# Optimization experiments

Measured on AMD Instinct MI355X. Metric: run time of the kernel, lower is better.

The kernel has to match this reference:

```python
import jax, jax.numpy as jnp
import numpy as np


def _gcn_layer(x, W, b, row, col, num_nodes):
    # x: [N, F_in]; W: [F_in, F_out]; row/col: [E2] (with self-loops appended)
    xw = x @ W  # [N, F_out]
    ones = jnp.ones(row.shape[0], dtype=xw.dtype)
    deg = jax.ops.segment_sum(ones, col, num_segments=num_nodes)  # in-degree incl. self-loop
    dinv = jnp.where(deg > 0, jax.lax.rsqrt(deg), 0.0)
    norm = dinv[row] * dinv[col]  # [E2]
    msg = xw[row] * norm[:, None]  # gather + per-edge scale
    out = jax.ops.segment_sum(msg, col, num_segments=num_nodes)  # scatter-add to targets
    return out + b


def setup_inputs() -> dict:
    key = jax.random.key(0)
    k1, k2, k3, k4, k5 = jax.random.split(key, 5)
    N, E, F_in, F_hid = 100000, 640000, 128, 128
    x = jax.random.normal(k1, (N, F_in), dtype=jnp.float32)
    edge_index = jax.random.randint(k2, (2, E), 0, N, dtype=jnp.int64)
    # Glorot-style init like PyG GCNConv
    s1 = (6.0 / (F_in + F_hid)) ** 0.5
    W1 = jax.random.uniform(k3, (F_in, F_hid), jnp.float32, -s1, s1)
    b1 = jnp.zeros((F_hid,), jnp.float32)
    s2 = (6.0 / (F_hid + F_hid)) ** 0.5
    W2 = jax.random.uniform(k4, (F_hid, F_hid), jnp.float32, -s2, s2)
    b2 = jnp.zeros((F_hid,), jnp.float32)
    return {"x": x, "edge_index": edge_index, "W1": W1, "b1": b1, "W2": W2, "b2": b2}


def reference(x, edge_index, W1, b1, W2, b2):
    N = x.shape[0]
    # GCN adds self-loops before symmetric normalization (add_self_loops=True default)
    self_idx = jnp.arange(N, dtype=edge_index.dtype)
    row = jnp.concatenate([edge_index[0], self_idx])
    col = jnp.concatenate([edge_index[1], self_idx])
    h = _gcn_layer(x, W1, b1, row, col, N)
    h = jax.nn.relu(h)
    # dropout is identity in eval mode (training=False)
    out = _gcn_layer(h, W2, b2, row, col, N)
    return out
```

## Files before the change

kernel.cpp:

```cpp
#include <hip/hip_runtime.h>
#include <cstdint>
#include <cstddef>


typedef unsigned int u32;
typedef unsigned short u16;
typedef __attribute__((ext_vector_type(8))) short short8;
typedef __attribute__((ext_vector_type(4))) float f32x4;

__device__ __forceinline__ float bf2f(u32 lo16) {
  union { u32 u; float f; } c; c.u = lo16 << 16; return c.f;
}
__device__ __forceinline__ u32 f2bf(float f) {
  union { float f; u32 u; } c; c.f = f;
  return (c.u + 0x7fffu + ((c.u >> 16) & 1u)) >> 16;
}

__global__ __launch_bounds__(256) void zero_i32_kernel(int* __restrict__ p, int n) {
  int i = blockIdx.x * 256 + threadIdx.x;
  if (i < n) p[i] = 0;
}

__global__ __launch_bounds__(256) void count_kernel(
    const int* __restrict__ cols, const int* __restrict__ rows,
    int* __restrict__ cnt, int E, int N) {
  int e = blockIdx.x * 256 + threadIdx.x;
  if (e >= E) return;
  int c = cols[e];
  int r = rows[e];
  if ((unsigned)c >= (unsigned)N || (unsigned)r >= (unsigned)N) return;
  atomicAdd(&cnt[c], 1);
}

__global__ __launch_bounds__(256) void wt_kernel(
    const float* __restrict__ W1, const float* __restrict__ W2,
    u16* __restrict__ Wt1, u16* __restrict__ Wt2) {
  int b = blockIdx.x;
  const float* W = (b < 64) ? W1 : W2;
  u16* Wt = (b < 64) ? Wt1 : Wt2;
  int idx = (b & 63) * 256 + threadIdx.x;
  int k = idx >> 7, n = idx & 127;
  Wt[n * 128 + k] = (u16)f2bf(W[idx]);
}

__global__ __launch_bounds__(256) void scan1_kernel(
    const int* __restrict__ cnt, int* __restrict__ rowptr,
    int* __restrict__ bsum, float* __restrict__ dinv, int N) {
  __shared__ int sd[256];
  int t = threadIdx.x;
  int base = blockIdx.x * 1024 + t * 4;
  int c0 = (base + 0 < N) ? cnt[base + 0] : 0;
  int c1 = (base + 1 < N) ? cnt[base + 1] : 0;
  int c2 = (base + 2 < N) ? cnt[base + 2] : 0;
  int c3 = (base + 3 < N) ? cnt[base + 3] : 0;
  if (base + 0 < N) dinv[base + 0] = rsqrtf((float)c0 + 1.0f);
  if (base + 1 < N) dinv[base + 1] = rsqrtf((float)c1 + 1.0f);
  if (base + 2 < N) dinv[base + 2] = rsqrtf((float)c2 + 1.0f);
  if (base + 3 < N) dinv[base + 3] = rsqrtf((float)c3 + 1.0f);
  int s = c0 + c1 + c2 + c3;
  sd[t] = s;
  __syncthreads();
  for (int off = 1; off < 256; off <<= 1) {
    int v = (t >= off) ? sd[t - off] : 0;
    __syncthreads();
    sd[t] += v;
    __syncthreads();
  }
  int excl = sd[t] - s;
  if (base + 0 < N) rowptr[base + 0] = excl;
  if (base + 1 < N) rowptr[base + 1] = excl + c0;
  if (base + 2 < N) rowptr[base + 2] = excl + c0 + c1;
  if (base + 3 < N) rowptr[base + 3] = excl + c0 + c1 + c2;
  if (t == 255) bsum[blockIdx.x] = sd[255];
}

__global__ __launch_bounds__(128) void scan2_kernel(
    const int* __restrict__ bsum, int* __restrict__ bsum2,
    int* __restrict__ rowptr, int NB, int N) {
  __shared__ int sd[128];
  int t = threadIdx.x;
  int v = (t < NB) ? bsum[t] : 0;
  sd[t] = v;
  __syncthreads();
  for (int off = 1; off < 128; off <<= 1) {
    int u = (t >= off) ? sd[t - off] : 0;
    __syncthreads();
    sd[t] += u;
    __syncthreads();
  }
  bsum2[t] = sd[t] - v;
  if (t == NB - 1) rowptr[N] = sd[t];
}

__global__ __launch_bounds__(256) void scan3_kernel(
    int* __restrict__ rowptr, const int* __restrict__ bsum2, int N) {
  int t = threadIdx.x;
  int b = blockIdx.x;
  int base = b * 1024 + t * 4;
  int add = bsum2[b];
#pragma unroll
  for (int k = 0; k < 4; k++)
    if (base + k < N) rowptr[base + k] += add;
}

__global__ __launch_bounds__(256) void fill_kernel(
    const int* __restrict__ cols, const int* __restrict__ rows,
    const int* __restrict__ rowptr, int* __restrict__ cnt,
    int* __restrict__ adj, int E, int N) {
  int e = blockIdx.x * 256 + threadIdx.x;
  if (e >= E) return;
  int c = cols[e];
  int r = rows[e];
  if ((unsigned)c >= (unsigned)N || (unsigned)r >= (unsigned)N) return;
  int pos = atomicSub(&cnt[c], 1) - 1;
  if (pos >= 0) adj[rowptr[c] + pos] = r;
}

template <int A_BF16>
__global__ __launch_bounds__(256) void gemm_mfma_kernel(
    const void* __restrict__ Av, const u16* __restrict__ Wt,
    const float* __restrict__ dinv, u16* __restrict__ C, int M) {
  __shared__ u16 Ws[128][136];
  __shared__ float dv_s[128];
  const int tid = threadIdx.x;
  const int row0 = blockIdx.x * 128;

  {
    const uint4* src = (const uint4*)Wt;
#pragma unroll
    for (int i = 0; i < 8; i++) {
      int linear = tid + i * 256;
      int n = linear >> 4;
      int kq = linear & 15;
      *(uint4*)&Ws[n][kq * 8] = src[linear];
    }
  }
  if (tid < 128) {
    int gr = row0 + tid;
    dv_s[tid] = (gr < M) ? dinv[gr] : 0.f;
  }
  __syncthreads();

  const int wave = tid >> 6;
  const int lane = tid & 63;
  const int lm = lane & 15;
  const int quad = lane >> 4;
  const int m0 = wave * 32;

  f32x4 acc[2][8];
#pragma unroll
  for (int mt = 0; mt < 2; mt++)
#pragma unroll
    for (int nt = 0; nt < 8; nt++) acc[mt][nt] = (f32x4){0.f, 0.f, 0.f, 0.f};

#pragma unroll
  for (int k0 = 0; k0 < 128; k0 += 32) {
    short8 bfrag[8];
#pragma unroll
    for (int nt = 0; nt < 8; nt++)
      bfrag[nt] = *(const short8*)&Ws[nt * 16 + lm][k0 + quad * 8];

    short8 afrag[2];
#pragma unroll
    for (int mt = 0; mt < 2; mt++) {
      int gr = row0 + m0 + mt * 16 + lm;
      short8 f = (short8){0, 0, 0, 0, 0, 0, 0, 0};
      if (gr < M) {
        if (A_BF16) {
          f = *(const short8*)((const u16*)Av + (size_t)gr * 128 + k0 + quad * 8);
        } else {
          const float* Af = (const float*)Av + (size_t)gr * 128 + k0 + quad * 8;
          float4 v0 = *(const float4*)Af;
          float4 v1 = *(const float4*)(Af + 4);
          f[0] = (short)f2bf(v0.x); f[1] = (short)f2bf(v0.y);
          f[2] = (short)f2bf(v0.z); f[3] = (short)f2bf(v0.w);
          f[4] = (short)f2bf(v1.x); f[5] = (short)f2bf(v1.y);
          f[6] = (short)f2bf(v1.z); f[7] = (short)f2bf(v1.w);
        }
      }
      afrag[mt] = f;
    }

#pragma unroll
    for (int mt = 0; mt < 2; mt++)
#pragma unroll
      for (int nt = 0; nt < 8; nt++)
        acc[mt][nt] = __builtin_amdgcn_mfma_f32_16x16x32_bf16(
            afrag[mt], bfrag[nt], acc[mt][nt], 0, 0, 0);
  }

  __syncthreads();
#pragma unroll
  for (int mt = 0; mt < 2; mt++) {
    int rbase = m0 + mt * 16 + quad * 4;
#pragma unroll
    for (int r = 0; r < 4; r++) {
      int lrow = rbase + r;
      float dv = dv_s[lrow];
#pragma unroll
      for (int nt = 0; nt < 8; nt++)
        Ws[lrow][nt * 16 + lm] = (u16)f2bf(acc[mt][nt][r] * dv);
    }
  }
  __syncthreads();
#pragma unroll
  for (int i = 0; i < 8; i++) {
    int linear = tid + i * 256;
    int row = linear >> 4;
    int c8 = linear & 15;
    int grow = row0 + row;
    if (grow < M)
      *(uint4*)(C + (size_t)grow * 128 + c8 * 8) = *(const uint4*)&Ws[row][c8 * 8];
  }
}

template <int RELU, int OUT_BF16>
__global__ __launch_bounds__(256) void aggregate_kernel(
    const uint4* __restrict__ xws, const int* __restrict__ rowptr,
    const int* __restrict__ adj, const float* __restrict__ dinv,
    const float* __restrict__ bias, void* __restrict__ out, int N) {
  int node = blockIdx.x * 16 + (threadIdx.x >> 4);
  if (node >= N) return;
  int lane = threadIdx.x & 15;

  float a[8];
  {
    uint4 sv = xws[(size_t)node * 16 + lane];
    a[0] = bf2f(sv.x & 0xffff); a[1] = bf2f(sv.x >> 16);
    a[2] = bf2f(sv.y & 0xffff); a[3] = bf2f(sv.y >> 16);
    a[4] = bf2f(sv.z & 0xffff); a[5] = bf2f(sv.z >> 16);
    a[6] = bf2f(sv.w & 0xffff); a[7] = bf2f(sv.w >> 16);
  }

  int beg = rowptr[node];
  int end = rowptr[node + 1];
  for (int j = beg; j < end; j += 8) {
    int sidx[8];
    float msk[8];
#pragma unroll
    for (int k = 0; k < 8; k++) {
      int jj = j + k;
      int s = (jj < end) ? adj[jj] : -1;
      float m = 1.f;
      if ((unsigned)s >= (unsigned)N) { s = 0; m = 0.f; }
      sidx[k] = s;
      msk[k] = m;
    }
    uint4 v[8];
#pragma unroll
    for (int k = 0; k < 8; k++) v[k] = xws[(size_t)sidx[k] * 16 + lane];
#pragma unroll
    for (int k = 0; k < 8; k++) {
      a[0] = fmaf(msk[k], bf2f(v[k].x & 0xffff), a[0]);
      a[1] = fmaf(msk[k], bf2f(v[k].x >> 16), a[1]);
      a[2] = fmaf(msk[k], bf2f(v[k].y & 0xffff), a[2]);
      a[3] = fmaf(msk[k], bf2f(v[k].y >> 16), a[3]);
      a[4] = fmaf(msk[k], bf2f(v[k].z & 0xffff), a[4]);
      a[5] = fmaf(msk[k], bf2f(v[k].z >> 16), a[5]);
      a[6] = fmaf(msk[k], bf2f(v[k].w & 0xffff), a[6]);
      a[7] = fmaf(msk[k], bf2f(v[k].w >> 16), a[7]);
    }
  }

  float di = dinv[node];
  float4 b0 = ((const float4*)bias)[lane * 2];
  float4 b1 = ((const float4*)bias)[lane * 2 + 1];
  float o[8];
  o[0] = fmaf(di, a[0], b0.x); o[1] = fmaf(di, a[1], b0.y);
  o[2] = fmaf(di, a[2], b0.z); o[3] = fmaf(di, a[3], b0.w);
  o[4] = fmaf(di, a[4], b1.x); o[5] = fmaf(di, a[5], b1.y);
  o[6] = fmaf(di, a[6], b1.z); o[7] = fmaf(di, a[7], b1.w);
  if (RELU) {
#pragma unroll
    for (int k = 0; k < 8; k++) o[k] = fmaxf(o[k], 0.f);
  }
  if (OUT_BF16) {
    uint4 p;
    p.x = f2bf(o[0]) | (f2bf(o[1]) << 16);
    p.y = f2bf(o[2]) | (f2bf(o[3]) << 16);
    p.z = f2bf(o[4]) | (f2bf(o[5]) << 16);
    p.w = f2bf(o[6]) | (f2bf(o[7]) << 16);
    ((uint4*)out)[(size_t)node * 16 + lane] = p;
  } else {
    float4* op = (float4*)out + (size_t)node * 32 + lane * 2;
    op[0] = make_float4(o[0], o[1], o[2], o[3]);
    op[1] = make_float4(o[4], o[5], o[6], o[7]);
  }
}

extern "C" void kernel_launch(void* const* d_in, const int* in_sizes, int n_in,
                              void* d_out, int out_size, void* d_ws, size_t ws_size,
                              hipStream_t stream) {
  const float* x  = (const float*)d_in[0];
  const int*   ei = (const int*)d_in[1];
  const float* W1 = (const float*)d_in[2];
  const float* b1 = (const float*)d_in[3];
  const float* W2 = (const float*)d_in[4];
  const float* b2 = (const float*)d_in[5];
  float* out = (float*)d_out;

  const int F = 128;
  const int N = in_sizes[0] / F;
  const int E = in_sizes[1] / 2;
  const int* rows = ei;
  const int* cols = ei + E;

  u16*   bufXW  = (u16*)d_ws;
  u16*   bufH   = bufXW + (size_t)N * F;
  float* dinv   = (float*)(bufH + (size_t)N * F);
  int*   cnt    = (int*)(dinv + N);
  int*   rowptr = cnt + N;
  int*   adj    = rowptr + (N + 1);
  int*   bsum   = adj + E;
  int*   bsum2  = bsum + 128;
  u16*   Wt1    = (u16*)(bsum2 + 128);
  u16*   Wt2    = Wt1 + 128 * 128;

  const int NB = (N + 1023) / 1024;
  int eblocks = (E + 255) / 256;
  int nblocks = (N + 255) / 256;

  zero_i32_kernel<<<nblocks, 256, 0, stream>>>(cnt, N);
  count_kernel<<<eblocks, 256, 0, stream>>>(cols, rows, cnt, E, N);
  wt_kernel<<<128, 256, 0, stream>>>(W1, W2, Wt1, Wt2);
  scan1_kernel<<<NB, 256, 0, stream>>>(cnt, rowptr, bsum, dinv, N);
  scan2_kernel<<<1, 128, 0, stream>>>(bsum, bsum2, rowptr, NB, N);
  scan3_kernel<<<NB, 256, 0, stream>>>(rowptr, bsum2, N);
  fill_kernel<<<eblocks, 256, 0, stream>>>(cols, rows, rowptr, cnt, adj, E, N);

  int gblocks = (N + 127) / 128;
  int ablocks = (N + 15) / 16;
  gemm_mfma_kernel<0><<<gblocks, 256, 0, stream>>>(x, Wt1, dinv, bufXW, N);
  aggregate_kernel<1, 1><<<ablocks, 256, 0, stream>>>(
      (const uint4*)bufXW, rowptr, adj, dinv, b1, bufH, N);
  gemm_mfma_kernel<1><<<gblocks, 256, 0, stream>>>(bufH, Wt2, dinv, bufXW, N);
  aggregate_kernel<0, 0><<<ablocks, 256, 0, stream>>>(
      (const uint4*)bufXW, rowptr, adj, dinv, b2, out, N);
}
```

Baseline: 261.9 us.

## Sort nodes into degree buckets before aggregation to balance warp work

Adds a degree histogram, a bucket scan and a counting-sort permutation so the aggregate kernels process nodes grouped by in-degree (capped at 31). Neighbouring 16-lane groups in a wavefront then have similar loop trip counts, which cuts divergence and idle lanes in the gather loop. The cost is three extra small kernel launches. Output rows are also written and self-features read in permuted order, which loses some locality for the output and self-row accesses.

```diff
diff --git a/kernel.cpp b/kernel.cpp
--- a/kernel.cpp
+++ b/kernel.cpp
@@ -76,9 +76,10 @@
 
 __global__ __launch_bounds__(128) void scan2_kernel(
     const int* __restrict__ bsum, int* __restrict__ bsum2,
-    int* __restrict__ rowptr, int NB, int N) {
+    int* __restrict__ rowptr, int* __restrict__ hist, int NB, int N) {
   __shared__ int sd[128];
   int t = threadIdx.x;
+  if (t < 32) hist[t] = 0;
   int v = (t < NB) ? bsum[t] : 0;
   sd[t] = v;
   __syncthreads();
@@ -114,6 +115,51 @@
   if ((unsigned)c >= (unsigned)N || (unsigned)r >= (unsigned)N) return;
   int pos = atomicSub(&cnt[c], 1) - 1;
   if (pos >= 0) adj[rowptr[c] + pos] = r;
+}
+
+__global__ __launch_bounds__(256) void hist_kernel(
+    const int* __restrict__ rowptr, int* __restrict__ hist, int N) {
+  __shared__ int lh[32];
+  int t = threadIdx.x;
+  if (t < 32) lh[t] = 0;
+  __syncthreads();
+  int i = blockIdx.x * 256 + t;
+  if (i < N) {
+    int deg = rowptr[i + 1] - rowptr[i];
+    int bin = deg < 31 ? deg : 31;
+    atomicAdd(&lh[bin], 1);
+  }
+  __syncthreads();
+  if (t < 32 && lh[t] > 0) atomicAdd(&hist[t], lh[t]);
+}
+
+__global__ __launch_bounds__(64) void binscan_kernel(
+    const int* __restrict__ hist, int* __restrict__ bincur) {
+  if (threadIdx.x == 0) {
+    int acc = 0;
+    for (int b = 0; b < 32; b++) { bincur[b] = acc; acc += hist[b]; }
+  }
+}
+
+__global__ __launch_bounds__(256) void perm_kernel(
+    const int* __restrict__ rowptr, int* __restrict__ bincur,
+    int* __restrict__ perm, int N) {
+  __shared__ int lh[32];
+  __shared__ int lbase[32];
+  int t = threadIdx.x;
+  if (t < 32) lh[t] = 0;
+  __syncthreads();
+  int i = blockIdx.x * 256 + t;
+  int bin = 0, lpos = 0;
+  if (i < N) {
+    int deg = rowptr[i + 1] - rowptr[i];
+    bin = deg < 31 ? deg : 31;
+    lpos = atomicAdd(&lh[bin], 1);
+  }
+  __syncthreads();
+  if (t < 32) lbase[t] = (lh[t] > 0) ? atomicAdd(&bincur[t], lh[t]) : 0;
+  __syncthreads();
+  if (i < N) perm[lbase[bin] + lpos] = i;
 }
 
 template <int A_BF16>
@@ -218,9 +264,12 @@
 __global__ __launch_bounds__(256) void aggregate_kernel(
     const uint4* __restrict__ xws, const int* __restrict__ rowptr,
     const int* __restrict__ adj, const float* __restrict__ dinv,
-    const float* __restrict__ bias, void* __restrict__ out, int N) {
-  int node = blockIdx.x * 16 + (threadIdx.x >> 4);
-  if (node >= N) return;
+    const float* __restrict__ bias, const int* __restrict__ perm,
+    void* __restrict__ out, int N) {
+  int idx = blockIdx.x * 16 + (threadIdx.x >> 4);
+  if (idx >= N) return;
+  int node = perm[idx];
+  if ((unsigned)node >= (unsigned)N) node = 0;
   int lane = threadIdx.x & 15;
 
   float a[8];
@@ -313,7 +362,10 @@
   int*   adj    = rowptr + (N + 1);
   int*   bsum   = adj + E;
   int*   bsum2  = bsum + 128;
-  u16*   Wt1    = (u16*)(bsum2 + 128);
+  int*   hist   = bsum2 + 128;
+  int*   bincur = hist + 32;
+  int*   perm   = bincur + 32;
+  u16*   Wt1    = (u16*)(perm + N);
   u16*   Wt2    = Wt1 + 128 * 128;
 
   const int NB = (N + 1023) / 1024;
@@ -324,16 +376,19 @@
   count_kernel<<<eblocks, 256, 0, stream>>>(cols, rows, cnt, E, N);
   wt_kernel<<<128, 256, 0, stream>>>(W1, W2, Wt1, Wt2);
   scan1_kernel<<<NB, 256, 0, stream>>>(cnt, rowptr, bsum, dinv, N);
-  scan2_kernel<<<1, 128, 0, stream>>>(bsum, bsum2, rowptr, NB, N);
+  scan2_kernel<<<1, 128, 0, stream>>>(bsum, bsum2, rowptr, hist, NB, N);
   scan3_kernel<<<NB, 256, 0, stream>>>(rowptr, bsum2, N);
   fill_kernel<<<eblocks, 256, 0, stream>>>(cols, rows, rowptr, cnt, adj, E, N);
+  hist_kernel<<<nblocks, 256, 0, stream>>>(rowptr, hist, N);
+  binscan_kernel<<<1, 64, 0, stream>>>(hist, bincur);
+  perm_kernel<<<nblocks, 256, 0, stream>>>(rowptr, bincur, perm, N);
 
   int gblocks = (N + 127) / 128;
   int ablocks = (N + 15) / 16;
   gemm_mfma_kernel<0><<<gblocks, 256, 0, stream>>>(x, Wt1, dinv, bufXW, N);
   aggregate_kernel<1, 1><<<ablocks, 256, 0, stream>>>(
-      (const uint4*)bufXW, rowptr, adj, dinv, b1, bufH, N);
+      (const uint4*)bufXW, rowptr, adj, dinv, b1, perm, bufH, N);
   gemm_mfma_kernel<1><<<gblocks, 256, 0, stream>>>(bufH, Wt2, dinv, bufXW, N);
   aggregate_kernel<0, 0><<<ablocks, 256, 0, stream>>>(
-      (const uint4*)bufXW, rowptr, adj, dinv, b2, out, N);
-}
+      (const uint4*)bufXW, rowptr, adj, dinv, b2, perm, out, N);
+}
```

After: 286.0 us. 9.2% more time.
